# Performance work log

Hardware: AMD Instinct MI355X
Metric: run time of the kernel (lower is better)

The kernel has to match this reference:

```python
import jax, jax.numpy as jnp
import numpy as np

N_HEADS = 8

def setup_inputs() -> dict:
    key = jax.random.key(0)
    ks = jax.random.split(key, 8)
    N, D, H = 20000, 16, 256
    scale = np.float32(0.02)
    return {
        "h": jax.random.normal(ks[0], (N, H), dtype=jnp.float32),
        "attention_mask": jnp.zeros((N,), dtype=jnp.float32),
        "neighbor_idx": jax.random.randint(ks[1], (N, D), 0, N, dtype=jnp.int32),
        "Wq": jax.random.normal(ks[2], (H, H), dtype=jnp.float32) * scale,
        "bq": jnp.zeros((H,), dtype=jnp.float32),
        "Wk": jax.random.normal(ks[3], (H, H), dtype=jnp.float32) * scale,
        "bk": jnp.zeros((H,), dtype=jnp.float32),
        "Wv": jax.random.normal(ks[4], (H, H), dtype=jnp.float32) * scale,
        "bv": jnp.zeros((H,), dtype=jnp.float32),
    }

def reference(h, attention_mask, neighbor_idx, Wq, bq, Wk, bk, Wv, bv):
    N, H = h.shape
    nh = N_HEADS
    dh = H // nh
    inv_sqrt_dh = np.float32(1.0 / np.sqrt(dh))
    # query from each node's own state: [N, nh, dh]
    q = (h @ Wq.T + bq).reshape(N, nh, dh)
    # gather neighbor mailbox: [N, D, H]
    nb = h[neighbor_idx]
    k = (nb @ Wk.T + bk).reshape(N, -1, nh, dh)  # [N, D, nh, dh]
    v = (nb @ Wv.T + bv).reshape(N, -1, nh, dh)
    # scores: [N, nh, D]
    scores = jnp.einsum('nhd,nkhd->nhk', q, k) * inv_sqrt_dh
    # additive mask gathered from source nodes, broadcast over heads
    scores = scores + attention_mask[neighbor_idx][:, None, :]
    probs = jax.nn.softmax(scores, axis=-1)
    # dropout prob = 0.0 (eval) -> identity
    ctx = jnp.einsum('nhk,nkhd->nhd', probs, v).reshape(N, H)
    return ctx
```

## Files before the change

### kernel.cpp

```cpp
#include <hip/hip_runtime.h>
#include <hip/hip_fp16.h>
#include <math.h>

#define HDIM 256
#define DNEIGH 16

typedef __attribute__((ext_vector_type(8))) short short8;
typedef __attribute__((ext_vector_type(4))) float f32x4;

static __device__ __forceinline__ unsigned short f2bf(float f) {
    unsigned int u = __float_as_uint(f);
    unsigned int r = (u + 0x7fffu + ((u >> 16) & 1u)) >> 16;
    return (unsigned short)r;
}
static __device__ __forceinline__ float bf_lo(unsigned int u) {
    return __uint_as_float(u << 16);
}
static __device__ __forceinline__ float bf_hi(unsigned int u) {
    return __uint_as_float(u & 0xffff0000u);
}

static __device__ __forceinline__ short8 pack8(float4 a, float4 b) {
    short8 o;
    o[0] = (short)f2bf(a.x); o[1] = (short)f2bf(a.y);
    o[2] = (short)f2bf(a.z); o[3] = (short)f2bf(a.w);
    o[4] = (short)f2bf(b.x); o[5] = (short)f2bf(b.y);
    o[6] = (short)f2bf(b.z); o[7] = (short)f2bf(b.w);
    return o;
}

#if __has_builtin(__builtin_amdgcn_cvt_pk_fp8_f32)
static __device__ __forceinline__ unsigned int fp8x4(float v0, float v1, float v2, float v3) {
    int p = __builtin_amdgcn_cvt_pk_fp8_f32(v0, v1, 0, false);
    p = __builtin_amdgcn_cvt_pk_fp8_f32(v2, v3, p, true);
    return (unsigned int)p;
}
#else
static __device__ __forceinline__ unsigned char f2fp8(float v) {
    unsigned short h = __half_as_ushort(__float2half(v * (1.0f / 256.0f)));
    unsigned short mag = h & 0x7fffu;
    mag = (unsigned short)((mag + 0x40u) >> 7);
    if (mag > 0x7f) mag = 0x7f;
    return (unsigned char)(((h >> 8) & 0x80u) | mag);
}
static __device__ __forceinline__ unsigned int fp8x4(float v0, float v1, float v2, float v3) {
    return (unsigned int)f2fp8(v0) | ((unsigned int)f2fp8(v1) << 8) |
           ((unsigned int)f2fp8(v2) << 16) | ((unsigned int)f2fp8(v3) << 24);
}
#endif

#if __has_builtin(__builtin_amdgcn_cvt_pk_f32_fp8)
#define HAVE_PK_DEC 1
#endif
#if __has_builtin(__builtin_amdgcn_cvt_f32_fp8)
#define FP8D(u, i) __builtin_amdgcn_cvt_f32_fp8((u), (i))
#else
static __device__ __forceinline__ float fp8_byte_dec(unsigned int b) {
    unsigned int hb = ((b & 0x80u) << 8) | ((b & 0x7fu) << 7);
    return __half2float(__ushort_as_half((unsigned short)hb)) * 256.0f;
}
#define FP8D(u, i) fp8_byte_dec(((u) >> ((i) * 8)) & 0xffu)
#endif

__global__ __launch_bounds__(256, 1) void qkv_fused_kernel(
    const float* __restrict__ h,
    const float* __restrict__ Wq, const float* __restrict__ Wk, const float* __restrict__ Wv,
    const float* __restrict__ bq, const float* __restrict__ bk, const float* __restrict__ bv,
    unsigned short* __restrict__ Qb, unsigned char* __restrict__ KV,
    int N)
{
    __shared__ unsigned short As[2][64 * 256];

    const int t = threadIdx.x;
    const int lane = t & 63;
    const int wid = t >> 6;
    const int sel = blockIdx.y;

    const float* __restrict__ W    = (sel == 0) ? Wq : (sel == 1) ? Wk : Wv;
    const float* __restrict__ bias = (sel == 0) ? bq : (sel == 1) ? bk : bv;
    const float wscale = (sel == 0) ? 0.17677669529663688f : 1.0f;

    const int ntiles = (N + 63) >> 6;
    const int BX = gridDim.x;

    const int srow = wid * 8 + (lane >> 3);
    const int tc = lane & 7;

    short8 af[8][4];
#pragma unroll
    for (int ks = 0; ks < 8; ++ks)
#pragma unroll
        for (int i = 0; i < 4; ++i) {
            int m = wid * 64 + i * 16 + (lane & 15);
            int cf = (ks * 4 + (lane >> 4)) * 8;
            float4 a = *(const float4*)&W[(size_t)m * 256 + cf];
            float4 b = *(const float4*)&W[(size_t)m * 256 + cf + 4];
            a.x *= wscale; a.y *= wscale; a.z *= wscale; a.w *= wscale;
            b.x *= wscale; b.y *= wscale; b.z *= wscale; b.w *= wscale;
            af[ks][i] = pack8(a, b);
        }

    float4 b4[4];
#pragma unroll
    for (int i = 0; i < 4; ++i) {
        int ch = wid * 64 + i * 16 + (lane >> 4) * 4;
        float4 bb = *(const float4*)&bias[ch];
        bb.x *= wscale; bb.y *= wscale; bb.z *= wscale; bb.w *= wscale;
        b4[i] = bb;
    }

    float4 fa[16];

    auto LOADA = [&](int tile0) {
#pragma unroll
        for (int s = 0; s < 2; ++s) {
            int gr = tile0 * 64 + s * 32 + srow;
            if (gr > N - 1) gr = N - 1;
            const float* hrow = &h[(size_t)gr * 256];
#pragma unroll
            for (int k = 0; k < 4; ++k) {
                fa[s * 8 + k * 2 + 0] = *(const float4*)&hrow[k * 64 + tc * 8];
                fa[s * 8 + k * 2 + 1] = *(const float4*)&hrow[k * 64 + tc * 8 + 4];
            }
        }
    };
    auto WRITEA = [&](int buf) {
#pragma unroll
        for (int s = 0; s < 2; ++s) {
            int r = s * 32 + srow;
#pragma unroll
            for (int k = 0; k < 4; ++k) {
                int c = k * 8 + tc;
                int pos = (c & ~7) | ((c ^ r) & 7);
                *(short8*)&As[buf][r * 256 + pos * 8] =
                    pack8(fa[s * 8 + k * 2], fa[s * 8 + k * 2 + 1]);
            }
        }
    };

    int tile = blockIdx.x;
    if (tile < ntiles) { LOADA(tile); WRITEA(0); }
    __syncthreads();

    for (int it = 0; tile < ntiles; ++it, tile += BX) {
        int cur = it & 1;
        int nxt_tile = tile + BX;
        bool havenext = nxt_tile < ntiles;
        if (havenext) LOADA(nxt_tile);

        f32x4 acc[4][4] = {};
#pragma unroll
        for (int ks = 0; ks < 8; ++ks) {
            short8 bf[4];
#pragma unroll
            for (int j = 0; j < 4; ++j) {
                int n = j * 16 + (lane & 15);
                int c = ks * 4 + (lane >> 4);
                int pos = (c & ~7) | ((c ^ n) & 7);
                bf[j] = *(const short8*)&As[cur][n * 256 + pos * 8];
            }
#pragma unroll
            for (int i = 0; i < 4; ++i)
#pragma unroll
                for (int j = 0; j < 4; ++j)
                    acc[i][j] = __builtin_amdgcn_mfma_f32_16x16x32_bf16(
                        af[ks][i], bf[j], acc[i][j], 0, 0, 0);
        }

        int nodeb = tile * 64;
#pragma unroll
        for (int i = 0; i < 4; ++i) {
            int ch = wid * 64 + i * 16 + (lane >> 4) * 4;
#pragma unroll
            for (int j = 0; j < 4; ++j) {
                int node = nodeb + j * 16 + (lane & 15);
                if (node < N) {
                    float v0 = acc[i][j][0] + b4[i].x;
                    float v1 = acc[i][j][1] + b4[i].y;
                    float v2 = acc[i][j][2] + b4[i].z;
                    float v3 = acc[i][j][3] + b4[i].w;
                    if (sel == 0) {
                        ushort4 o;
                        o.x = f2bf(v0); o.y = f2bf(v1); o.z = f2bf(v2); o.w = f2bf(v3);
                        *(ushort4*)&Qb[(size_t)node * HDIM + ch] = o;
                    } else if (sel == 1) {
                        *(unsigned int*)&KV[(size_t)node * 768 + ch] = fp8x4(v0, v1, v2, v3);
                    } else {
                        ushort4 o;
                        o.x = f2bf(v0); o.y = f2bf(v1); o.z = f2bf(v2); o.w = f2bf(v3);
                        *(ushort4*)&KV[(size_t)node * 768 + 256 + (size_t)ch * 2] = o;
                    }
                }
            }
        }

        if (havenext) WRITEA(cur ^ 1);
        __syncthreads();
    }
}

__global__ __launch_bounds__(256) void attn4_kernel(
    const unsigned short* __restrict__ Qb,
    const unsigned char* __restrict__ KV,
    const float* __restrict__ mask,
    const int* __restrict__ nidx,
    float* __restrict__ out,
    int N)
{
    const int w = threadIdx.x >> 6;
    const int lane = threadIdx.x & 63;
    const int n = blockIdx.x * 4 + w;
    if (n >= N) return;

    int idl = nidx[(size_t)n * DNEIGH + (lane & 15)];
    float mskl = mask[idl];

    unsigned int kreg[DNEIGH];
    uint2 vreg[DNEIGH];
#pragma unroll
    for (int d = 0; d < DNEIGH; ++d) {
        int id = __builtin_amdgcn_readlane(idl, d);
        const unsigned char* kv = &KV[(size_t)id * 768];
        kreg[d] = *(const unsigned int*)(kv + lane * 4);
        vreg[d] = *(const uint2*)(kv + 256 + lane * 8);
    }

    uint2 qu = *(const uint2*)&Qb[(size_t)n * HDIM + lane * 4];
    const float q0 = bf_lo(qu.x), q1 = bf_hi(qu.x);
    const float q2 = bf_lo(qu.y), q3 = bf_hi(qu.y);

    float e[DNEIGH];
    float s = 0.f;
#pragma unroll
    for (int d = 0; d < DNEIGH; ++d) {
        float pdot;
#ifdef HAVE_PK_DEC
        auto k01 = __builtin_amdgcn_cvt_pk_f32_fp8((int)kreg[d], false);
        auto k23 = __builtin_amdgcn_cvt_pk_f32_fp8((int)kreg[d], true);
        pdot = q0 * k01[0] + q1 * k01[1] + q2 * k23[0] + q3 * k23[1];
#else
        pdot = q0 * FP8D(kreg[d], 0) + q1 * FP8D(kreg[d], 1)
             + q2 * FP8D(kreg[d], 2) + q3 * FP8D(kreg[d], 3);
#endif
        pdot += __shfl_xor(pdot, 1);
        pdot += __shfl_xor(pdot, 2);
        pdot += __shfl_xor(pdot, 4);
        float mk = __int_as_float(__builtin_amdgcn_readlane(__float_as_int(mskl), d));
        e[d] = __expf(pdot + mk);
        s += e[d];
    }
    float rs = 1.f / s;

    float4 acc = make_float4(0.f, 0.f, 0.f, 0.f);
#pragma unroll
    for (int d = 0; d < DNEIGH; ++d) {
        float wgt = e[d] * rs;
        acc.x += wgt * bf_lo(vreg[d].x);
        acc.y += wgt * bf_hi(vreg[d].x);
        acc.z += wgt * bf_lo(vreg[d].y);
        acc.w += wgt * bf_hi(vreg[d].y);
    }
    *(float4*)&out[(size_t)n * HDIM + lane * 4] = acc;
}

extern "C" void kernel_launch(void* const* d_in, const int* in_sizes, int n_in,
                              void* d_out, int out_size, void* d_ws, size_t ws_size,
                              hipStream_t stream)
{
    const float* h    = (const float*)d_in[0];
    const float* mask = (const float*)d_in[1];
    const int*   nidx = (const int*)d_in[2];
    const float* Wq   = (const float*)d_in[3];
    const float* bq   = (const float*)d_in[4];
    const float* Wk   = (const float*)d_in[5];
    const float* bk   = (const float*)d_in[6];
    const float* Wv   = (const float*)d_in[7];
    const float* bv   = (const float*)d_in[8];

    const int N = in_sizes[0] / HDIM;

    char* ws = (char*)d_ws;
    unsigned short* Qbp = (unsigned short*)ws; ws += (size_t)N * HDIM * 2;
    unsigned char*  KVp = (unsigned char*)ws;

    dim3 g1(84, 3);
    qkv_fused_kernel<<<g1, 256, 0, stream>>>(h, Wq, Wk, Wv, bq, bk, bv, Qbp, KVp, N);

    attn4_kernel<<<(N + 3) / 4, 256, 0, stream>>>(Qbp, KVp, mask, nidx, (float*)d_out, N);
}
```

Measured before the change: 141.0 us.

## Interleave K/V per lane in KV buffer and use packed bf16 conversion

```diff
diff --git a/kernel.cpp b/kernel.cpp
--- a/kernel.cpp
+++ b/kernel.cpp
@@ -20,12 +20,20 @@
     return __uint_as_float(u & 0xffff0000u);
 }
 
-static __device__ __forceinline__ short8 pack8(float4 a, float4 b) {
-    short8 o;
-    o[0] = (short)f2bf(a.x); o[1] = (short)f2bf(a.y);
-    o[2] = (short)f2bf(a.z); o[3] = (short)f2bf(a.w);
-    o[4] = (short)f2bf(b.x); o[5] = (short)f2bf(b.y);
-    o[6] = (short)f2bf(b.z); o[7] = (short)f2bf(b.w);
+static __device__ __forceinline__ unsigned int cvtpk(float lo, float hi) {
+    unsigned int r;
+    asm("v_cvt_pk_bf16_f32 %0, %1, %2" : "=v"(r) : "v"(lo), "v"(hi));
+    return r;
+}
+
+union U4S8 { uint4 u; short8 s; };
+
+static __device__ __forceinline__ uint4 pack8u(float4 a, float4 b) {
+    uint4 o;
+    o.x = cvtpk(a.x, a.y);
+    o.y = cvtpk(a.z, a.w);
+    o.z = cvtpk(b.x, b.y);
+    o.w = cvtpk(b.z, b.w);
     return o;
 }
 
@@ -97,7 +105,8 @@
             float4 b = *(const float4*)&W[(size_t)m * 256 + cf + 4];
             a.x *= wscale; a.y *= wscale; a.z *= wscale; a.w *= wscale;
             b.x *= wscale; b.y *= wscale; b.z *= wscale; b.w *= wscale;
-            af[ks][i] = pack8(a, b);
+            U4S8 u; u.u = pack8u(a, b);
+            af[ks][i] = u.s;
         }
 
     float4 b4[4];
@@ -132,8 +141,8 @@
             for (int k = 0; k < 4; ++k) {
                 int c = k * 8 + tc;
                 int pos = (c & ~7) | ((c ^ r) & 7);
-                *(short8*)&As[buf][r * 256 + pos * 8] =
-                    pack8(fa[s * 8 + k * 2], fa[s * 8 + k * 2 + 1]);
+                *(uint4*)&As[buf][r * 256 + pos * 8] =
+                    pack8u(fa[s * 8 + k * 2], fa[s * 8 + k * 2 + 1]);
             }
         }
     };
@@ -171,6 +180,7 @@
 #pragma unroll
         for (int i = 0; i < 4; ++i) {
             int ch = wid * 64 + i * 16 + (lane >> 4) * 4;
+            int g  = ch >> 2;
 #pragma unroll
             for (int j = 0; j < 4; ++j) {
                 int node = nodeb + j * 16 + (lane & 15);
@@ -180,15 +190,15 @@
                     float v2 = acc[i][j][2] + b4[i].z;
                     float v3 = acc[i][j][3] + b4[i].w;
                     if (sel == 0) {
-                        ushort4 o;
-                        o.x = f2bf(v0); o.y = f2bf(v1); o.z = f2bf(v2); o.w = f2bf(v3);
-                        *(ushort4*)&Qb[(size_t)node * HDIM + ch] = o;
+                        *(uint2*)&Qb[(size_t)node * HDIM + ch] =
+                            make_uint2(cvtpk(v0, v1), cvtpk(v2, v3));
                     } else if (sel == 1) {
-                        *(unsigned int*)&KV[(size_t)node * 768 + ch] = fp8x4(v0, v1, v2, v3);
+                        *(unsigned int*)&KV[(size_t)node * 768 + g * 12] =
+                            fp8x4(v0, v1, v2, v3);
                     } else {
-                        ushort4 o;
-                        o.x = f2bf(v0); o.y = f2bf(v1); o.z = f2bf(v2); o.w = f2bf(v3);
-                        *(ushort4*)&KV[(size_t)node * 768 + 256 + (size_t)ch * 2] = o;
+                        unsigned char* p = &KV[(size_t)node * 768 + g * 12 + 4];
+                        *(unsigned int*)p       = cvtpk(v0, v1);
+                        *(unsigned int*)(p + 4) = cvtpk(v2, v3);
                     }
                 }
             }
@@ -215,14 +225,14 @@
     int idl = nidx[(size_t)n * DNEIGH + (lane & 15)];
     float mskl = mask[idl];
 
-    unsigned int kreg[DNEIGH];
-    uint2 vreg[DNEIGH];
+    unsigned int ka[DNEIGH], vb[DNEIGH], vc[DNEIGH];
 #pragma unroll
     for (int d = 0; d < DNEIGH; ++d) {
         int id = __builtin_amdgcn_readlane(idl, d);
-        const unsigned char* kv = &KV[(size_t)id * 768];
-        kreg[d] = *(const unsigned int*)(kv + lane * 4);
-        vreg[d] = *(const uint2*)(kv + 256 + lane * 8);
+        const unsigned char* p = &KV[(size_t)id * 768 + lane * 12];
+        ka[d] = *(const unsigned int*)p;
+        vb[d] = *(const unsigned int*)(p + 4);
+        vc[d] = *(const unsigned int*)(p + 8);
     }
 
     uint2 qu = *(const uint2*)&Qb[(size_t)n * HDIM + lane * 4];
@@ -235,12 +245,12 @@
     for (int d = 0; d < DNEIGH; ++d) {
         float pdot;
 #ifdef HAVE_PK_DEC
-        auto k01 = __builtin_amdgcn_cvt_pk_f32_fp8((int)kreg[d], false);
-        auto k23 = __builtin_amdgcn_cvt_pk_f32_fp8((int)kreg[d], true);
+        auto k01 = __builtin_amdgcn_cvt_pk_f32_fp8((int)ka[d], false);
+        auto k23 = __builtin_amdgcn_cvt_pk_f32_fp8((int)ka[d], true);
         pdot = q0 * k01[0] + q1 * k01[1] + q2 * k23[0] + q3 * k23[1];
 #else
-        pdot = q0 * FP8D(kreg[d], 0) + q1 * FP8D(kreg[d], 1)
-             + q2 * FP8D(kreg[d], 2) + q3 * FP8D(kreg[d], 3);
+        pdot = q0 * FP8D(ka[d], 0) + q1 * FP8D(ka[d], 1)
+             + q2 * FP8D(ka[d], 2) + q3 * FP8D(ka[d], 3);
 #endif
         pdot += __shfl_xor(pdot, 1);
         pdot += __shfl_xor(pdot, 2);
@@ -255,10 +265,10 @@
 #pragma unroll
     for (int d = 0; d < DNEIGH; ++d) {
         float wgt = e[d] * rs;
-        acc.x += wgt * bf_lo(vreg[d].x);
-        acc.y += wgt * bf_hi(vreg[d].x);
-        acc.z += wgt * bf_lo(vreg[d].y);
-        acc.w += wgt * bf_hi(vreg[d].y);
+        acc.x += wgt * bf_lo(vb[d]);
+        acc.y += wgt * bf_hi(vb[d]);
+        acc.z += wgt * bf_lo(vc[d]);
+        acc.w += wgt * bf_hi(vc[d]);
     }
     *(float4*)&out[(size_t)n * HDIM + lane * 4] = acc;
 }
```

New measurement: 141.6 us. About the same (+0.4%).
